# Kernel optimization log

Hardware: AMD Instinct MI355X
Metric: run time of the kernel (lower is better)

Reference implementation:

```python
import jax, jax.numpy as jnp
import numpy as np

B, LX, LY, D = 8, 2048, 2048, 256

def setup_inputs() -> dict:
    key = jax.random.key(0)
    k1, k2, k3, k4 = jax.random.split(key, 4)
    x = jax.random.normal(k1, (B, LX, D), dtype=jnp.float32)
    y = jax.random.normal(k2, (B, LY, D), dtype=jnp.float32)
    y_mask = jax.random.randint(k3, (B, LY), 0, 2).astype(jnp.bool_)
    W = jax.random.normal(k4, (D, D), dtype=jnp.float32) * (1.0 / np.sqrt(D))
    b = jnp.zeros((D,), dtype=jnp.float32)
    return {"x": x, "y": y, "y_mask": y_mask, "W": W, "b": b}

def reference(x, y, y_mask, W, b):
    # shared linear + relu projection (torch Linear: x @ W.T + b)
    x_proj = jax.nn.relu(jnp.einsum('bld,ed->ble', x, W) + b)  # [B,LX,D]
    y_proj = jax.nn.relu(jnp.einsum('bld,ed->ble', y, W) + b)  # [B,LY,D]
    scores = jnp.einsum('bxd,byd->bxy', x_proj, y_proj)        # [B,LX,LY]
    scores = jnp.where(y_mask[:, None, :], -jnp.inf, scores)
    alpha = jax.nn.softmax(scores, axis=-1)                    # [B,LX,LY]
    return jnp.einsum('bxy,byd->bxd', alpha, y)                # [B,LX,D]
```

## Files before the change

kernel.cpp:

```cpp
#include <hip/hip_runtime.h>

typedef __attribute__((ext_vector_type(8))) short short8;
typedef _Float16 half8 __attribute__((ext_vector_type(8)));
typedef __attribute__((ext_vector_type(4))) float f32x4;
typedef __attribute__((ext_vector_type(4))) unsigned int uint4v;
typedef __attribute__((ext_vector_type(2))) unsigned int uint2v;

#define B_   8
#define LX_  2048
#define LY_  2048
#define D_   256
#define NROW (B_ * LX_)

__device__ __forceinline__ unsigned short f2bf(float f) {
  unsigned u = __builtin_bit_cast(unsigned, f);
  u += 0x7FFF + ((u >> 16) & 1);
  return (unsigned short)(u >> 16);
}
__device__ __forceinline__ float bf2f(unsigned short h) {
  unsigned u = ((unsigned)h) << 16;
  return __builtin_bit_cast(float, u);
}

__global__ __launch_bounds__(256) void prep_kernel(
    const float* __restrict__ W, unsigned short* __restrict__ Whi,
    unsigned short* __restrict__ Wlo,
    const int* __restrict__ MASK, int* __restrict__ CIDX, int* __restrict__ Lc) {
  int t = threadIdx.x;
  if (blockIdx.x >= 8) {
    int base = (blockIdx.x - 8) * 2048 + t * 8;
    f32x4 f0 = *(const f32x4*)(W + base);
    f32x4 f1 = *(const f32x4*)(W + base + 4);
    float v[8] = {f0[0], f0[1], f0[2], f0[3], f1[0], f1[1], f1[2], f1[3]};
    unsigned short h[8], l[8];
    for (int j = 0; j < 8; ++j) {
      h[j] = f2bf(v[j]);
      l[j] = f2bf(v[j] - bf2f(h[j]));
    }
    uint4v vh = {(unsigned)h[0] | ((unsigned)h[1] << 16), (unsigned)h[2] | ((unsigned)h[3] << 16),
                 (unsigned)h[4] | ((unsigned)h[5] << 16), (unsigned)h[6] | ((unsigned)h[7] << 16)};
    uint4v vl = {(unsigned)l[0] | ((unsigned)l[1] << 16), (unsigned)l[2] | ((unsigned)l[3] << 16),
                 (unsigned)l[4] | ((unsigned)l[5] << 16), (unsigned)l[6] | ((unsigned)l[7] << 16)};
    *(uint4v*)(Whi + base) = vh;
    *(uint4v*)(Wlo + base) = vl;
    return;
  }
  __shared__ int s[256];
  int b = blockIdx.x;
  int f[8];
  int cnt = 0;
  for (int k = 0; k < 8; ++k) {
    f[k] = (MASK[b * 2048 + t * 8 + k] == 0) ? 1 : 0;
    cnt += f[k];
  }
  s[t] = cnt;
  __syncthreads();
  for (int off = 1; off < 256; off <<= 1) {
    int v = (t >= off) ? s[t - off] : 0;
    __syncthreads();
    s[t] += v;
    __syncthreads();
  }
  if (t == 255) Lc[b] = s[255];
  int off = s[t] - cnt;
  for (int k = 0; k < 8; ++k) {
    int j = t * 8 + k;
    if (f[k]) CIDX[b * 2048 + (off++)] = j;
  }
}

__global__ __launch_bounds__(256, 2) void projgather_kernel(
    const float* __restrict__ X, const float* __restrict__ Y,
    const float* __restrict__ bias,
    const unsigned short* __restrict__ Whi, const unsigned short* __restrict__ Wlo,
    const int* __restrict__ CIDX, const int* __restrict__ Lc,
    _Float16* __restrict__ XP, _Float16* __restrict__ YPc,
    _Float16* __restrict__ YTc) {
  __shared__ __align__(16) unsigned char smem[51200];
  int t = threadIdx.x;

  if (blockIdx.x >= 512) {
    _Float16 (*tile)[72] = (_Float16(*)[72])smem;
    int id = blockIdx.x - 512;
    int db = id & 3, nb = (id >> 2) & 31, b = id >> 7;
    int lc = Lc[b];
    int end = (lc + 31) & ~31;
    if (nb * 64 >= end) return;
    int nl = t >> 2, ds = t & 3;
    int j = nb * 64 + nl;
    int idx = (j < lc) ? CIDX[b * 2048 + j] : 0;
    const float* src = Y + (size_t)(b * LY_ + idx) * D_ + db * 64 + ds * 16;
    for (int i = 0; i < 4; ++i) {
      f32x4 f = *(const f32x4*)(src + i * 4);
      for (int k = 0; k < 4; ++k) tile[ds * 16 + i * 4 + k][nl] = (_Float16)f[k];
    }
    __syncthreads();
    int dl = t >> 2, nsub = t & 3;
    uint4v v0 = *(const uint4v*)&tile[dl][nsub * 16];
    uint4v v1 = *(const uint4v*)&tile[dl][nsub * 16 + 8];
    _Float16* dst = YTc + (size_t)(b * D_ + db * 64 + dl) * LY_ + nb * 64 + nsub * 16;
    *(uint4v*)(dst) = v0;
    *(uint4v*)(dst + 8) = v1;
    return;
  }

  unsigned short (*Ah)[40] = (unsigned short(*)[40])(smem);
  unsigned short (*Al)[40] = (unsigned short(*)[40])(smem + 5120);
  unsigned short (*Bh)[40] = (unsigned short(*)[40])(smem + 10240);
  unsigned short (*Bl)[40] = (unsigned short(*)[40])(smem + 30720);

  int lane = t & 63, wave = t >> 6;
  int q = lane >> 4, n15 = lane & 15;
  int arow = t >> 2, aseg = t & 3;
  int erow = t >> 2, ec = t & 3;

  bool isX = blockIdx.x < 256;
  int m0 = 0, b = 0, slot0 = 0, lcb = 0;
  const float* arow_ptr;
  if (isX) {
    m0 = blockIdx.x * 64;
    arow_ptr = X + (size_t)(m0 + arow) * D_;
  } else {
    int id = blockIdx.x - 256;
    b = id >> 5;
    int rb = id & 31;
    lcb = Lc[b];
    slot0 = rb * 64;
    if (slot0 >= lcb) return;
    int sl = slot0 + arow;
    int grow = (sl < lcb) ? CIDX[b * 2048 + sl] : 0;
    arow_ptr = Y + (size_t)(b * 2048 + grow) * D_;
  }

  f32x4 acc[4][4];
  for (int mt = 0; mt < 4; ++mt)
    for (int nt = 0; nt < 4; ++nt) acc[mt][nt] = (f32x4){0.f, 0.f, 0.f, 0.f};

  f32x4 pa[2];
  uint4v pbh[4], pbl[4];
#define PROJ_PF(kc)                                                            \
  {                                                                            \
    for (int i = 0; i < 2; ++i)                                                \
      pa[i] = *(const f32x4*)(arow_ptr + (kc) * 32 + (aseg + i * 4) * 4);      \
    for (int p = 0; p < 4; ++p) {                                              \
      int e = p * 64 + erow;                                                   \
      pbh[p] = *(const uint4v*)(Whi + (size_t)e * D_ + (kc) * 32 + ec * 8);    \
      pbl[p] = *(const uint4v*)(Wlo + (size_t)e * D_ + (kc) * 32 + ec * 8);    \
    }                                                                          \
  }

  PROJ_PF(0);

  for (int kc = 0; kc < 8; ++kc) {
    __syncthreads();
    for (int i = 0; i < 2; ++i) {
      int seg = aseg + i * 4;
      f32x4 f = pa[i];
      unsigned short h[4], l[4];
      for (int j = 0; j < 4; ++j) {
        h[j] = f2bf(f[j]);
        l[j] = f2bf(f[j] - bf2f(h[j]));
      }
      uint2v vh = {(unsigned)h[0] | ((unsigned)h[1] << 16),
                   (unsigned)h[2] | ((unsigned)h[3] << 16)};
      uint2v vl = {(unsigned)l[0] | ((unsigned)l[1] << 16),
                   (unsigned)l[2] | ((unsigned)l[3] << 16)};
      *(uint2v*)&Ah[arow][seg * 4] = vh;
      *(uint2v*)&Al[arow][seg * 4] = vl;
    }
    for (int p = 0; p < 4; ++p) {
      int e = p * 64 + erow;
      *(uint4v*)&Bh[e][ec * 8] = pbh[p];
      *(uint4v*)&Bl[e][ec * 8] = pbl[p];
    }
    if (kc < 7) PROJ_PF(kc + 1);
    __syncthreads();

    short8 afh[4], afl[4], bfh[4], bfl[4];
    for (int mt = 0; mt < 4; ++mt) {
      afh[mt] = *(const short8*)&Ah[mt * 16 + n15][q * 8];
      afl[mt] = *(const short8*)&Al[mt * 16 + n15][q * 8];
    }
    for (int nt = 0; nt < 4; ++nt) {
      bfh[nt] = *(const short8*)&Bh[wave * 64 + nt * 16 + n15][q * 8];
      bfl[nt] = *(const short8*)&Bl[wave * 64 + nt * 16 + n15][q * 8];
    }
    for (int mt = 0; mt < 4; ++mt)
      for (int nt = 0; nt < 4; ++nt) {
        acc[mt][nt] = __builtin_amdgcn_mfma_f32_16x16x32_bf16(afh[mt], bfh[nt], acc[mt][nt], 0, 0, 0);
        acc[mt][nt] = __builtin_amdgcn_mfma_f32_16x16x32_bf16(afl[mt], bfh[nt], acc[mt][nt], 0, 0, 0);
        acc[mt][nt] = __builtin_amdgcn_mfma_f32_16x16x32_bf16(afh[mt], bfl[nt], acc[mt][nt], 0, 0, 0);
      }
  }
#undef PROJ_PF

  __syncthreads();
  _Float16 (*epi)[264] = (_Float16(*)[264])smem;
  for (int nt = 0; nt < 4; ++nt) {
    int e = wave * 64 + nt * 16 + n15;
    float bv = bias[e];
    for (int mt = 0; mt < 4; ++mt)
      for (int r = 0; r < 4; ++r) {
        float v = acc[mt][nt][r] + bv;
        v = v > 0.f ? v : 0.f;
        epi[mt * 16 + q * 4 + r][e] = (_Float16)v;
      }
  }
  __syncthreads();
  int row = t >> 2, seg = t & 3;
  bool valid = isX || (slot0 + row < lcb);
  if (valid) {
    _Float16* drp = isX ? (XP + (size_t)(m0 + row) * D_)
                        : (YPc + (size_t)(b * 2048 + slot0 + row) * D_);
    for (int k = 0; k < 8; ++k) {
      uint4v v = *(const uint4v*)&epi[row][seg * 64 + k * 8];
      *(uint4v*)(drp + seg * 64 + k * 8) = v;
    }
  }
}

__global__ __launch_bounds__(256, 2) void flash_kernel(
    const _Float16* __restrict__ XP, const _Float16* __restrict__ YPc,
    const _Float16* __restrict__ YTc, const int* __restrict__ Lc,
    _Float16* __restrict__ PO, float* __restrict__ Pm, float* __restrict__ Pl) {
  __shared__ __align__(16) _Float16 yp_t[64][264];
  __shared__ __align__(16) _Float16 yT_t[256][64];
  __shared__ __align__(16) _Float16 pbuf[4][16][72];

  int t = threadIdx.x;
  int lane = t & 63, wave = t >> 6;
  int q = lane >> 4, n15 = lane & 15;
  int wg = (int)blockIdx.x;
  int swz = (wg & 7) * 64 + (wg >> 3);
  int half = swz & 1;
  int xb = (swz >> 1) & 31;
  int b = swz >> 6;
  int row0 = xb * 64 + wave * 16;

  int lc = Lc[b];
  int T  = (lc + 63) >> 6;
  int tstart = (T * half) >> 1;
  int tend   = (T * (half + 1)) >> 1;

  half8 a[8];
  const _Float16* xrow = XP + (size_t)(b * LX_ + row0 + n15) * D_ + q * 8;
  for (int kk = 0; kk < 8; ++kk) a[kk] = *(const half8*)(xrow + kk * 32);

  float m_r[4];
  for (int r = 0; r < 4; ++r) m_r[r] = -1e30f;
  f32x4 lacc = {0.f, 0.f, 0.f, 0.f};
  f32x4 oacc[16];
  for (int dt = 0; dt < 16; ++dt) oacc[dt] = (f32x4){0.f, 0.f, 0.f, 0.f};

  const _Float16* ypb = YPc + (size_t)b * LY_ * D_;
  const _Float16* yTb = YTc + (size_t)b * D_ * LY_;

  uint4v pr[16];
#define PREFETCH(tt)                                                          \
  {                                                                           \
    int y0p = (tt) * 64;                                                      \
    for (int i = 0; i < 8; ++i) {                                             \
      int c = t + i * 256;                                                    \
      pr[i] = *(const uint4v*)(ypb + (size_t)(y0p + (c >> 5)) * D_ + (c & 31) * 8); \
    }                                                                         \
    for (int i = 0; i < 8; ++i) {                                             \
      int c = t + i * 256;                                                    \
      pr[8 + i] = *(const uint4v*)(yTb + (size_t)(c >> 3) * LY_ + y0p + (c & 7) * 8); \
    }                                                                         \
  }

  if (tstart < tend) PREFETCH(tstart);

  for (int tt = tstart; tt < tend; ++tt) {
    int y0 = tt * 64;
    __syncthreads();
    for (int i = 0; i < 8; ++i) {
      int c = t + i * 256;
      *(uint4v*)&yp_t[c >> 5][(c & 31) * 8] = pr[i];
    }
    for (int i = 0; i < 8; ++i) {
      int c = t + i * 256;
      int rT = c >> 3, pc = (c & 7) ^ (rT & 7);
      *(uint4v*)&yT_t[rT][pc * 8] = pr[8 + i];
    }
    if (tt + 1 < tend) PREFETCH(tt + 1);
    __syncthreads();

    f32x4 S0 = {0.f, 0.f, 0.f, 0.f}, S1 = {0.f, 0.f, 0.f, 0.f};
    f32x4 S2 = {0.f, 0.f, 0.f, 0.f}, S3 = {0.f, 0.f, 0.f, 0.f};
    for (int kk = 0; kk < 8; ++kk) {
      half8 b0 = *(const half8*)&yp_t[n15][kk * 32 + q * 8];
      half8 b1 = *(const half8*)&yp_t[16 + n15][kk * 32 + q * 8];
      half8 b2 = *(const half8*)&yp_t[32 + n15][kk * 32 + q * 8];
      half8 b3 = *(const half8*)&yp_t[48 + n15][kk * 32 + q * 8];
      S0 = __builtin_amdgcn_mfma_f32_16x16x32_f16(a[kk], b0, S0, 0, 0, 0);
      S1 = __builtin_amdgcn_mfma_f32_16x16x32_f16(a[kk], b1, S1, 0, 0, 0);
      S2 = __builtin_amdgcn_mfma_f32_16x16x32_f16(a[kk], b2, S2, 0, 0, 0);
      S3 = __builtin_amdgcn_mfma_f32_16x16x32_f16(a[kk], b3, S3, 0, 0, 0);
    }
    bool mk0 = (y0 + n15) >= lc;
    bool mk1 = (y0 + 16 + n15) >= lc;
    bool mk2 = (y0 + 32 + n15) >= lc;
    bool mk3 = (y0 + 48 + n15) >= lc;

    f32x4 alv;
    bool need = false;
#pragma unroll
    for (int r = 0; r < 4; ++r) {
      float s0 = mk0 ? -1e30f : S0[r];
      float s1 = mk1 ? -1e30f : S1[r];
      float s2 = mk2 ? -1e30f : S2[r];
      float s3 = mk3 ? -1e30f : S3[r];
      float tm = fmaxf(fmaxf(s0, s1), fmaxf(s2, s3));
      tm = fmaxf(tm, __shfl_xor(tm, 1));
      tm = fmaxf(tm, __shfl_xor(tm, 2));
      tm = fmaxf(tm, __shfl_xor(tm, 4));
      tm = fmaxf(tm, __shfl_xor(tm, 8));
      float mn = fmaxf(m_r[r], tm);
      float al = __expf(m_r[r] - mn);
      m_r[r] = mn;
      float p0 = __expf(s0 - mn);
      float p1 = __expf(s1 - mn);
      float p2 = __expf(s2 - mn);
      float p3 = __expf(s3 - mn);
      pbuf[wave][q * 4 + r][n15]      = (_Float16)p0;
      pbuf[wave][q * 4 + r][16 + n15] = (_Float16)p1;
      pbuf[wave][q * 4 + r][32 + n15] = (_Float16)p2;
      pbuf[wave][q * 4 + r][48 + n15] = (_Float16)p3;
      lacc[r] = lacc[r] * al + (p0 + p1) + (p2 + p3);
      alv[r] = al;
      need = need || (al != 1.0f);
    }
    if (__ballot(need)) {
      for (int dt = 0; dt < 16; ++dt)
        for (int r = 0; r < 4; ++r) oacc[dt][r] *= alv[r];
    }
    half8 pa0 = *(const half8*)&pbuf[wave][n15][q * 8];
    half8 pa1 = *(const half8*)&pbuf[wave][n15][32 + q * 8];
    for (int dt = 0; dt < 16; ++dt) {
      int rT = dt * 16 + n15, x = rT & 7;
      half8 bb0 = *(const half8*)&yT_t[rT][(q ^ x) * 8];
      half8 bb1 = *(const half8*)&yT_t[rT][((4 + q) ^ x) * 8];
      oacc[dt] = __builtin_amdgcn_mfma_f32_16x16x32_f16(pa0, bb0, oacc[dt], 0, 0, 0);
      oacc[dt] = __builtin_amdgcn_mfma_f32_16x16x32_f16(pa1, bb1, oacc[dt], 0, 0, 0);
    }
  }
#undef PREFETCH

  size_t prow = (size_t)(half * B_ + b) * LX_ + row0;
  _Float16* po = PO + prow * D_;
  for (int dt = 0; dt < 16; ++dt)
    for (int r = 0; r < 4; ++r)
      po[(size_t)(q * 4 + r) * D_ + dt * 16 + n15] = (_Float16)oacc[dt][r];
  for (int r = 0; r < 4; ++r) {
    float v = lacc[r];
    v += __shfl_xor(v, 1);
    v += __shfl_xor(v, 2);
    v += __shfl_xor(v, 4);
    v += __shfl_xor(v, 8);
    lacc[r] = v;
  }
  if (n15 == 0) {
    for (int r = 0; r < 4; ++r) {
      Pm[prow + q * 4 + r] = m_r[r];
      Pl[prow + q * 4 + r] = lacc[r];
    }
  }
}

__global__ __launch_bounds__(256) void merge_kernel(
    const _Float16* __restrict__ PO, const float* __restrict__ Pm,
    const float* __restrict__ Pl, float* __restrict__ OUT) {
  int c = blockIdx.x * 256 + threadIdx.x;
  int row = c >> 5, seg = c & 31;
  float m0 = Pm[row], m1 = Pm[NROW + row];
  float l0 = Pl[row], l1 = Pl[NROW + row];
  float m = fmaxf(m0, m1);
  float w0 = __expf(m0 - m), w1 = __expf(m1 - m);
  float inv = 1.0f / (l0 * w0 + l1 * w1);
  const _Float16* p0 = PO + (size_t)row * D_ + seg * 8;
  const _Float16* p1 = p0 + (size_t)NROW * D_;
  half8 a = *(const half8*)p0;
  half8 bsec = *(const half8*)p1;
  float* o = OUT + (size_t)row * D_ + seg * 8;
  f32x4 o0, o1;
  for (int j = 0; j < 4; ++j) o0[j] = ((float)a[j] * w0 + (float)bsec[j] * w1) * inv;
  for (int j = 0; j < 4; ++j) o1[j] = ((float)a[4 + j] * w0 + (float)bsec[4 + j] * w1) * inv;
  *(f32x4*)o = o0;
  *(f32x4*)(o + 4) = o1;
}

extern "C" void kernel_launch(void* const* d_in, const int* in_sizes, int n_in,
                              void* d_out, int out_size, void* d_ws, size_t ws_size,
                              hipStream_t stream) {
  const float* x     = (const float*)d_in[0];
  const float* y     = (const float*)d_in[1];
  const int*   ymask = (const int*)  d_in[2];
  const float* W     = (const float*)d_in[3];
  const float* bias  = (const float*)d_in[4];
  float* out = (float*)d_out;

  char* ws = (char*)d_ws;
  size_t o = 0;
  unsigned short* Whi = (unsigned short*)(ws + o); o += 131072;
  unsigned short* Wlo = (unsigned short*)(ws + o); o += 131072;
  _Float16* XP  = (_Float16*)(ws + o); o += 8388608;
  _Float16* YPc = (_Float16*)(ws + o); o += 8388608;
  _Float16* YTc = (_Float16*)(ws + o); o += 8388608;
  _Float16* PO  = (_Float16*)(ws + o); o += 16777216;
  float* Pm   = (float*)(ws + o); o += 131072;
  float* Pl   = (float*)(ws + o); o += 131072;
  int*   CIDX = (int*)  (ws + o); o += 65536;
  int*   Lc   = (int*)  (ws + o);

  prep_kernel<<<40, 256, 0, stream>>>(W, Whi, Wlo, ymask, CIDX, Lc);
  projgather_kernel<<<1536, 256, 0, stream>>>(x, y, bias, Whi, Wlo, CIDX, Lc,
                                              XP, YPc, YTc);
  flash_kernel<<<512, 256, 0, stream>>>(XP, YPc, YTc, Lc, PO, Pm, Pl);
  merge_kernel<<<2048, 256, 0, stream>>>(PO, Pm, Pl, out);
}
```

Before: 152.4 us.

## Fuse compacted Y transpose into projection blocks, reusing loaded Y rows

Drops the separate transpose blocks that re-read gathered Y rows from global memory. Instead, the projection blocks for Y keep the fp16 copies of the rows they already loaded in registers, then transpose them through shared memory and write them to YTc. This removes a second pass over the compacted Y data and cuts the grid from 1536 to 512 blocks. In exchange it holds 32 extra registers per thread under a two-blocks-per-CU launch bound, which risks spills or lower occupancy. The K loop is also fully unrolled so the register array can be indexed statically.

```diff
diff --git a/kernel.cpp b/kernel.cpp
--- a/kernel.cpp
+++ b/kernel.cpp
@@ -78,31 +78,6 @@
     _Float16* __restrict__ YTc) {
   __shared__ __align__(16) unsigned char smem[51200];
   int t = threadIdx.x;
-
-  if (blockIdx.x >= 512) {
-    _Float16 (*tile)[72] = (_Float16(*)[72])smem;
-    int id = blockIdx.x - 512;
-    int db = id & 3, nb = (id >> 2) & 31, b = id >> 7;
-    int lc = Lc[b];
-    int end = (lc + 31) & ~31;
-    if (nb * 64 >= end) return;
-    int nl = t >> 2, ds = t & 3;
-    int j = nb * 64 + nl;
-    int idx = (j < lc) ? CIDX[b * 2048 + j] : 0;
-    const float* src = Y + (size_t)(b * LY_ + idx) * D_ + db * 64 + ds * 16;
-    for (int i = 0; i < 4; ++i) {
-      f32x4 f = *(const f32x4*)(src + i * 4);
-      for (int k = 0; k < 4; ++k) tile[ds * 16 + i * 4 + k][nl] = (_Float16)f[k];
-    }
-    __syncthreads();
-    int dl = t >> 2, nsub = t & 3;
-    uint4v v0 = *(const uint4v*)&tile[dl][nsub * 16];
-    uint4v v1 = *(const uint4v*)&tile[dl][nsub * 16 + 8];
-    _Float16* dst = YTc + (size_t)(b * D_ + db * 64 + dl) * LY_ + nb * 64 + nsub * 16;
-    *(uint4v*)(dst) = v0;
-    *(uint4v*)(dst + 8) = v1;
-    return;
-  }
 
   unsigned short (*Ah)[40] = (unsigned short(*)[40])(smem);
   unsigned short (*Al)[40] = (unsigned short(*)[40])(smem + 5120);
@@ -136,6 +111,8 @@
   for (int mt = 0; mt < 4; ++mt)
     for (int nt = 0; nt < 4; ++nt) acc[mt][nt] = (f32x4){0.f, 0.f, 0.f, 0.f};
 
+  half8 yraw[8];
+
   f32x4 pa[2];
   uint4v pbh[4], pbl[4];
 #define PROJ_PF(kc)                                                            \
@@ -151,11 +128,17 @@
 
   PROJ_PF(0);
 
+#pragma unroll
   for (int kc = 0; kc < 8; ++kc) {
     __syncthreads();
+#pragma unroll
     for (int i = 0; i < 2; ++i) {
       int seg = aseg + i * 4;
       f32x4 f = pa[i];
+      if (!isX) {
+#pragma unroll
+        for (int j = 0; j < 4; ++j) yraw[kc][i * 4 + j] = (_Float16)f[j];
+      }
       unsigned short h[4], l[4];
       for (int j = 0; j < 4; ++j) {
         h[j] = f2bf(f[j]);
@@ -215,6 +198,29 @@
     for (int k = 0; k < 8; ++k) {
       uint4v v = *(const uint4v*)&epi[row][seg * 64 + k * 8];
       *(uint4v*)(drp + seg * 64 + k * 8) = v;
+    }
+  }
+
+  if (!isX) {
+    __syncthreads();
+    _Float16 (*t2)[72] = (_Float16(*)[72])smem;
+#pragma unroll
+    for (int kc = 0; kc < 8; ++kc) {
+#pragma unroll
+      for (int i = 0; i < 2; ++i)
+#pragma unroll
+        for (int j = 0; j < 4; ++j) {
+          int col = kc * 32 + (aseg + i * 4) * 4 + j;
+          t2[col][arow] = yraw[kc][i * 4 + j];
+        }
+    }
+    __syncthreads();
+    for (int p = 0; p < 4; ++p) {
+      int d = p * 64 + (t >> 2);
+      const _Float16* src2 = &t2[d][(t & 3) * 16];
+      _Float16* dst = YTc + (size_t)(b * D_ + d) * LY_ + slot0 + (t & 3) * 16;
+      *(uint4v*)(dst) = *(const uint4v*)(src2);
+      *(uint4v*)(dst + 8) = *(const uint4v*)(src2 + 8);
     }
   }
 }
@@ -414,8 +420,8 @@
   int*   Lc   = (int*)  (ws + o);
 
   prep_kernel<<<40, 256, 0, stream>>>(W, Whi, Wlo, ymask, CIDX, Lc);
-  projgather_kernel<<<1536, 256, 0, stream>>>(x, y, bias, Whi, Wlo, CIDX, Lc,
-                                              XP, YPc, YTc);
+  projgather_kernel<<<512, 256, 0, stream>>>(x, y, bias, Whi, Wlo, CIDX, Lc,
+                                             XP, YPc, YTc);
   flash_kernel<<<512, 256, 0, stream>>>(XP, YPc, YTc, Lc, PO, Pm, Pl);
   merge_kernel<<<2048, 256, 0, stream>>>(PO, Pm, Pl, out);
 }
```

Result: no change. 153.7 us (+0.9%).

## Fuse split-K merge into flash kernel using two wave-groups per block

Applied to the files above, without the earlier changes.

The two halves of the key range are now handled by two 4-wave groups inside one 512-thread block, each with its own shared-memory tile buffers. The partial outputs and row statistics are combined through shared memory at the end, and the result is written straight to the output. This removes the separate merge kernel and the global partial-output round trip. In exchange it doubles shared memory per block and raises the thread count per block, which may reduce occupancy. Both groups also synchronise at every iteration, so one may idle when the tile counts differ.

```diff
diff --git a/kernel.cpp b/kernel.cpp
--- a/kernel.cpp
+++ b/kernel.cpp
@@ -219,28 +219,31 @@
   }
 }
 
-__global__ __launch_bounds__(256, 2) void flash_kernel(
+__global__ __launch_bounds__(512, 2) void flashout_kernel(
     const _Float16* __restrict__ XP, const _Float16* __restrict__ YPc,
     const _Float16* __restrict__ YTc, const int* __restrict__ Lc,
-    _Float16* __restrict__ PO, float* __restrict__ Pm, float* __restrict__ Pl) {
-  __shared__ __align__(16) _Float16 yp_t[64][264];
-  __shared__ __align__(16) _Float16 yT_t[256][64];
-  __shared__ __align__(16) _Float16 pbuf[4][16][72];
+    float* __restrict__ OUT) {
+  __shared__ __align__(16) _Float16 yp_t[2][64][264];
+  __shared__ __align__(16) _Float16 yT_t[2][256][64];
+  __shared__ __align__(16) _Float16 pbuf[8][16][72];
 
   int t = threadIdx.x;
   int lane = t & 63, wave = t >> 6;
+  int g = wave >> 2;
+  int wv = wave & 3;
+  int tl = t & 255;
   int q = lane >> 4, n15 = lane & 15;
   int wg = (int)blockIdx.x;
-  int swz = (wg & 7) * 64 + (wg >> 3);
-  int half = swz & 1;
-  int xb = (swz >> 1) & 31;
-  int b = swz >> 6;
-  int row0 = xb * 64 + wave * 16;
+  int swz = (wg & 7) * 32 + (wg >> 3);
+  int xb = swz & 31;
+  int b = swz >> 5;
+  int row0 = xb * 64 + wv * 16;
 
   int lc = Lc[b];
   int T  = (lc + 63) >> 6;
-  int tstart = (T * half) >> 1;
-  int tend   = (T * (half + 1)) >> 1;
+  int tstart = (T * g) >> 1;
+  int tend   = (T * (g + 1)) >> 1;
+  int nit    = T - (T >> 1);
 
   half8 a[8];
   const _Float16* xrow = XP + (size_t)(b * LX_ + row0 + n15) * D_ + q * 8;
@@ -260,39 +263,44 @@
   {                                                                           \
     int y0p = (tt) * 64;                                                      \
     for (int i = 0; i < 8; ++i) {                                             \
-      int c = t + i * 256;                                                    \
+      int c = tl + i * 256;                                                   \
       pr[i] = *(const uint4v*)(ypb + (size_t)(y0p + (c >> 5)) * D_ + (c & 31) * 8); \
     }                                                                         \
     for (int i = 0; i < 8; ++i) {                                             \
-      int c = t + i * 256;                                                    \
+      int c = tl + i * 256;                                                   \
       pr[8 + i] = *(const uint4v*)(yTb + (size_t)(c >> 3) * LY_ + y0p + (c & 7) * 8); \
     }                                                                         \
   }
 
   if (tstart < tend) PREFETCH(tstart);
 
-  for (int tt = tstart; tt < tend; ++tt) {
+  for (int it = 0; it < nit; ++it) {
+    int tt = tstart + it;
+    bool val = tt < tend;
     int y0 = tt * 64;
     __syncthreads();
-    for (int i = 0; i < 8; ++i) {
-      int c = t + i * 256;
-      *(uint4v*)&yp_t[c >> 5][(c & 31) * 8] = pr[i];
-    }
-    for (int i = 0; i < 8; ++i) {
-      int c = t + i * 256;
-      int rT = c >> 3, pc = (c & 7) ^ (rT & 7);
-      *(uint4v*)&yT_t[rT][pc * 8] = pr[8 + i];
-    }
-    if (tt + 1 < tend) PREFETCH(tt + 1);
-    __syncthreads();
+    if (val) {
+      for (int i = 0; i < 8; ++i) {
+        int c = tl + i * 256;
+        *(uint4v*)&yp_t[g][c >> 5][(c & 31) * 8] = pr[i];
+      }
+      for (int i = 0; i < 8; ++i) {
+        int c = tl + i * 256;
+        int rT = c >> 3, pc = (c & 7) ^ (rT & 7);
+        *(uint4v*)&yT_t[g][rT][pc * 8] = pr[8 + i];
+      }
+      if (tt + 1 < tend) PREFETCH(tt + 1);
+    }
+    __syncthreads();
+    if (!val) continue;
 
     f32x4 S0 = {0.f, 0.f, 0.f, 0.f}, S1 = {0.f, 0.f, 0.f, 0.f};
     f32x4 S2 = {0.f, 0.f, 0.f, 0.f}, S3 = {0.f, 0.f, 0.f, 0.f};
     for (int kk = 0; kk < 8; ++kk) {
-      half8 b0 = *(const half8*)&yp_t[n15][kk * 32 + q * 8];
-      half8 b1 = *(const half8*)&yp_t[16 + n15][kk * 32 + q * 8];
-      half8 b2 = *(const half8*)&yp_t[32 + n15][kk * 32 + q * 8];
-      half8 b3 = *(const half8*)&yp_t[48 + n15][kk * 32 + q * 8];
+      half8 b0 = *(const half8*)&yp_t[g][n15][kk * 32 + q * 8];
+      half8 b1 = *(const half8*)&yp_t[g][16 + n15][kk * 32 + q * 8];
+      half8 b2 = *(const half8*)&yp_t[g][32 + n15][kk * 32 + q * 8];
+      half8 b3 = *(const half8*)&yp_t[g][48 + n15][kk * 32 + q * 8];
       S0 = __builtin_amdgcn_mfma_f32_16x16x32_f16(a[kk], b0, S0, 0, 0, 0);
       S1 = __builtin_amdgcn_mfma_f32_16x16x32_f16(a[kk], b1, S1, 0, 0, 0);
       S2 = __builtin_amdgcn_mfma_f32_16x16x32_f16(a[kk], b2, S2, 0, 0, 0);
@@ -339,19 +347,14 @@
     half8 pa1 = *(const half8*)&pbuf[wave][n15][32 + q * 8];
     for (int dt = 0; dt < 16; ++dt) {
       int rT = dt * 16 + n15, x = rT & 7;
-      half8 bb0 = *(const half8*)&yT_t[rT][(q ^ x) * 8];
-      half8 bb1 = *(const half8*)&yT_t[rT][((4 + q) ^ x) * 8];
+      half8 bb0 = *(const half8*)&yT_t[g][rT][(q ^ x) * 8];
+      half8 bb1 = *(const half8*)&yT_t[g][rT][((4 + q) ^ x) * 8];
       oacc[dt] = __builtin_amdgcn_mfma_f32_16x16x32_f16(pa0, bb0, oacc[dt], 0, 0, 0);
       oacc[dt] = __builtin_amdgcn_mfma_f32_16x16x32_f16(pa1, bb1, oacc[dt], 0, 0, 0);
     }
   }
 #undef PREFETCH
 
-  size_t prow = (size_t)(half * B_ + b) * LX_ + row0;
-  _Float16* po = PO + prow * D_;
-  for (int dt = 0; dt < 16; ++dt)
-    for (int r = 0; r < 4; ++r)
-      po[(size_t)(q * 4 + r) * D_ + dt * 16 + n15] = (_Float16)oacc[dt][r];
   for (int r = 0; r < 4; ++r) {
     float v = lacc[r];
     v += __shfl_xor(v, 1);
@@ -360,34 +363,36 @@
     v += __shfl_xor(v, 8);
     lacc[r] = v;
   }
-  if (n15 == 0) {
+
+  __syncthreads();
+  _Float16 (*Obuf)[256] = (_Float16(*)[256])&yp_t[0][0][0];
+  float (*ml)[2] = (float(*)[2])&yT_t[0][0][0];
+  if (g == 1) {
+    for (int dt = 0; dt < 16; ++dt)
+      for (int r = 0; r < 4; ++r)
+        Obuf[wv * 16 + q * 4 + r][dt * 16 + n15] = (_Float16)oacc[dt][r];
+    if (n15 == 0)
+      for (int r = 0; r < 4; ++r) {
+        ml[wv * 16 + q * 4 + r][0] = m_r[r];
+        ml[wv * 16 + q * 4 + r][1] = lacc[r];
+      }
+  }
+  __syncthreads();
+  if (g == 0) {
     for (int r = 0; r < 4; ++r) {
-      Pm[prow + q * 4 + r] = m_r[r];
-      Pl[prow + q * 4 + r] = lacc[r];
-    }
-  }
-}
-
-__global__ __launch_bounds__(256) void merge_kernel(
-    const _Float16* __restrict__ PO, const float* __restrict__ Pm,
-    const float* __restrict__ Pl, float* __restrict__ OUT) {
-  int c = blockIdx.x * 256 + threadIdx.x;
-  int row = c >> 5, seg = c & 31;
-  float m0 = Pm[row], m1 = Pm[NROW + row];
-  float l0 = Pl[row], l1 = Pl[NROW + row];
-  float m = fmaxf(m0, m1);
-  float w0 = __expf(m0 - m), w1 = __expf(m1 - m);
-  float inv = 1.0f / (l0 * w0 + l1 * w1);
-  const _Float16* p0 = PO + (size_t)row * D_ + seg * 8;
-  const _Float16* p1 = p0 + (size_t)NROW * D_;
-  half8 a = *(const half8*)p0;
-  half8 bsec = *(const half8*)p1;
-  float* o = OUT + (size_t)row * D_ + seg * 8;
-  f32x4 o0, o1;
-  for (int j = 0; j < 4; ++j) o0[j] = ((float)a[j] * w0 + (float)bsec[j] * w1) * inv;
-  for (int j = 0; j < 4; ++j) o1[j] = ((float)a[4 + j] * w0 + (float)bsec[4 + j] * w1) * inv;
-  *(f32x4*)o = o0;
-  *(f32x4*)(o + 4) = o1;
+      int rl = wv * 16 + q * 4 + r;
+      float m1 = ml[rl][0], l1 = ml[rl][1];
+      float m0 = m_r[r], l0 = lacc[r];
+      float mm = fmaxf(m0, m1);
+      float w0 = __expf(m0 - mm), w1 = __expf(m1 - mm);
+      float inv = 1.0f / (l0 * w0 + l1 * w1);
+      float* orow = OUT + (size_t)(b * LX_ + xb * 64 + rl) * D_;
+      for (int dt = 0; dt < 16; ++dt) {
+        float o1 = (float)Obuf[rl][dt * 16 + n15];
+        orow[dt * 16 + n15] = (oacc[dt][r] * w0 + o1 * w1) * inv;
+      }
+    }
+  }
 }
 
 extern "C" void kernel_launch(void* const* d_in, const int* in_sizes, int n_in,
@@ -407,15 +412,11 @@
   _Float16* XP  = (_Float16*)(ws + o); o += 8388608;
   _Float16* YPc = (_Float16*)(ws + o); o += 8388608;
   _Float16* YTc = (_Float16*)(ws + o); o += 8388608;
-  _Float16* PO  = (_Float16*)(ws + o); o += 16777216;
-  float* Pm   = (float*)(ws + o); o += 131072;
-  float* Pl   = (float*)(ws + o); o += 131072;
   int*   CIDX = (int*)  (ws + o); o += 65536;
   int*   Lc   = (int*)  (ws + o);
 
   prep_kernel<<<40, 256, 0, stream>>>(W, Whi, Wlo, ymask, CIDX, Lc);
   projgather_kernel<<<1536, 256, 0, stream>>>(x, y, bias, Whi, Wlo, CIDX, Lc,
                                               XP, YPc, YTc);
-  flash_kernel<<<512, 256, 0, stream>>>(XP, YPc, YTc, Lc, PO, Pm, Pl);
-  merge_kernel<<<2048, 256, 0, stream>>>(PO, Pm, Pl, out);
-}
+  flashout_kernel<<<256, 512, 0, stream>>>(XP, YPc, YTc, Lc, out);
+}
```

After: 148.1 us. -2.8%, faster.
